# Kernel optimization log

Hardware: AMD Instinct MI355X
Metric: run time of the kernel (lower is better)

## Reference

```python
import jax, jax.numpy as jnp
import numpy as np

N = 100000
H = 512
E = 8
EPS = 1e-12


def _xavier(key, fan_out, fan_in):
    a = float(np.sqrt(6.0 / (fan_in + fan_out)))
    return jax.random.uniform(key, (fan_out, fan_in), jnp.float32, -a, a)


def setup_inputs() -> dict:
    key = jax.random.key(0)
    ks = jax.random.split(key, 5)
    return {
        "x": jax.random.normal(ks[0], (N, H), jnp.float32),
        "Wq": _xavier(ks[1], H, H), "bq": jnp.zeros((H,), jnp.float32),
        "Wk": _xavier(ks[2], H, H), "bk": jnp.zeros((H,), jnp.float32),
        "Wv": _xavier(ks[3], H, H), "bv": jnp.zeros((H,), jnp.float32),
        "We": _xavier(ks[4], E, H), "be": jnp.zeros((E,), jnp.float32),
    }


def reference(x, Wq, bq, Wk, bk, Wv, bv, We, be):
    n = x.shape[0]
    q = x @ Wq.T + bq                      # [N,H]
    k = x @ Wk.T + bk                      # [N,H]
    v = x @ Wv.T + bv                      # [N,H]
    q = q / jnp.maximum(jnp.linalg.norm(q), EPS)   # Frobenius norm scaling
    k = k / jnp.maximum(jnp.linalg.norm(k), EPS)
    k_sum = jnp.sum(k, axis=0)             # k^T @ ones -> [H]
    attn_norm = 1.0 + (q @ k_sum)[:, None] / n     # [N,1]
    kv = k.T @ v                           # [H,H] associative trick
    global_repr = v + (q @ kv) / n         # [N,H]
    global_repr = global_repr / jnp.maximum(attn_norm, EPS)
    global_logits = global_repr @ We.T + be        # [N,E]
    return (global_repr, global_logits)
```

## Files before the change

kernel.cpp:

```cpp
#include <hip/hip_runtime.h>
#include <hip/hip_bf16.h>
#include <stdint.h>

#define Nrows 100000
#define Hdim  512
#define Edim  8


typedef float f32x4 __attribute__((ext_vector_type(4)));
typedef short bfrag __attribute__((ext_vector_type(8)));
typedef unsigned short u16;
typedef unsigned short u16x4 __attribute__((ext_vector_type(4)));

__device__ __forceinline__ u16 f2bf(float f) {
  union { float f; uint32_t u; } v; v.f = f;
  return (u16)((v.u + 0x7FFFu + ((v.u >> 16) & 1u)) >> 16);
}
__device__ __forceinline__ float waveReduce(float p) {
  #pragma unroll
  for (int off = 32; off > 0; off >>= 1) p += __shfl_down(p, off);
  return p;
}
__device__ __forceinline__ int permA(int r) {
  return (r & 1) | ((r & 2) << 1) | ((r & 4) >> 1);
}

__global__ __launch_bounds__(256) void kPrep(
    const float* __restrict__ Wv, const float* __restrict__ bv,
    const float* __restrict__ We, const float* __restrict__ be,
    u16* __restrict__ Bfin, float* __restrict__ b2e) {
  int b = blockIdx.x, t = threadIdx.x, lane = t & 63, wid = t >> 6;
  if (b < 8) {
    __shared__ float wes[512];
    for (int j = t; j < 512; j += 256) wes[j] = We[(size_t)b * Hdim + j];
    __syncthreads();
    float a0 = 0.f, a1 = 0.f;
    for (int j = 0; j < 512; ++j) {
      float w = wes[j];
      a0 += w * Wv[(size_t)j * Hdim + t];
      a1 += w * Wv[(size_t)j * Hdim + t + 256];
    }
    Bfin[(size_t)(512 + b) * Hdim + t]       = f2bf(a0);
    Bfin[(size_t)(512 + b) * Hdim + t + 256] = f2bf(a1);
    if (wid == 0) {
      float p = 0.f;
      for (int j = lane; j < 512; j += 64) p += wes[j] * bv[j];
      p = waveReduce(p);
      if (lane == 0) b2e[512 + b] = p + be[b];
    }
  } else {
    int c = b - 8;
    #pragma unroll 4
    for (int i = 0; i < 32; ++i) {
      int idx = c * 32768 + i * 1024 + t * 4;
      float4 v = *(const float4*)(Wv + idx);
      u16x4 o = { f2bf(v.x), f2bf(v.y), f2bf(v.z), f2bf(v.w) };
      *(u16x4*)(Bfin + idx) = o;
    }
    if (c == 0) { b2e[t] = bv[t]; b2e[t + 256] = bv[t + 256]; }
  }
}

__global__ __launch_bounds__(256, 2) void kMain(
    const float* __restrict__ x, const u16* __restrict__ Bfin,
    const float* __restrict__ b2e, float* __restrict__ out) {
  extern __shared__ char smem[];
  u16* __restrict__ Alds = (u16*)smem;
  u16* __restrict__ Blds = (u16*)(smem + 65536);
  const int t = threadIdx.x, lane = t & 63, wid = t >> 6;
  const int wm = wid >> 1, wc = wid & 1;
  const int l15 = lane & 15, l16 = lane >> 4;
  const int m0 = blockIdx.x * 64;

  const int a_row = t >> 2, a_c = t & 3;
  const int a_perm = permA(a_row);
  int arg = m0 + a_row; if (arg > Nrows - 1) arg = Nrows - 1;
  const float* xrow = x + (size_t)arg * Hdim;

  const int b_row = t >> 1, b_p = t & 1;
  const int b_xor = b_row & 7;

  float4 ra0, ra1, ra2, ra3; bfrag rb0, rb1, rb2, rb3;
  ra0 = *(const float4*)(xrow + a_c * 8);
  ra1 = *(const float4*)(xrow + a_c * 8 + 4);
  ra2 = *(const float4*)(xrow + (a_c + 4) * 8);
  ra3 = *(const float4*)(xrow + (a_c + 4) * 8 + 4);
  {
    const u16* bp = Bfin + (size_t)b_row * Hdim + b_p * 32;
    rb0 = *(const bfrag*)bp;        rb1 = *(const bfrag*)(bp + 8);
    rb2 = *(const bfrag*)(bp + 16); rb3 = *(const bfrag*)(bp + 24);
  }

  f32x4 acc[2][4] = {};
  for (int s = 0; s < 32; ++s) {
    const int nt = s >> 3, kt = s & 7;
    __syncthreads();
    if (nt == 0) {
      bfrag w0, w1;
      w0[0] = (short)f2bf(ra0.x); w0[1] = (short)f2bf(ra0.y);
      w0[2] = (short)f2bf(ra0.z); w0[3] = (short)f2bf(ra0.w);
      w0[4] = (short)f2bf(ra1.x); w0[5] = (short)f2bf(ra1.y);
      w0[6] = (short)f2bf(ra1.z); w0[7] = (short)f2bf(ra1.w);
      w1[0] = (short)f2bf(ra2.x); w1[1] = (short)f2bf(ra2.y);
      w1[2] = (short)f2bf(ra2.z); w1[3] = (short)f2bf(ra2.w);
      w1[4] = (short)f2bf(ra3.x); w1[5] = (short)f2bf(ra3.y);
      w1[6] = (short)f2bf(ra3.z); w1[7] = (short)f2bf(ra3.w);
      *(bfrag*)&Alds[a_row * 512 + (kt * 8 + (a_c ^ a_perm)) * 8] = w0;
      *(bfrag*)&Alds[a_row * 512 + (kt * 8 + ((a_c + 4) ^ a_perm)) * 8] = w1;
    }
    *(bfrag*)&Blds[b_row * 64 + (((b_p * 4 + 0) ^ b_xor) * 8)] = rb0;
    *(bfrag*)&Blds[b_row * 64 + (((b_p * 4 + 1) ^ b_xor) * 8)] = rb1;
    *(bfrag*)&Blds[b_row * 64 + (((b_p * 4 + 2) ^ b_xor) * 8)] = rb2;
    *(bfrag*)&Blds[b_row * 64 + (((b_p * 4 + 3) ^ b_xor) * 8)] = rb3;
    if (s < 31) {
      const int s1 = s + 1, nt1 = s1 >> 3, kt1 = s1 & 7;
      if (s1 < 8) {
        const float* xp = xrow + kt1 * 64;
        ra0 = *(const float4*)(xp + a_c * 8);
        ra1 = *(const float4*)(xp + a_c * 8 + 4);
        ra2 = *(const float4*)(xp + (a_c + 4) * 8);
        ra3 = *(const float4*)(xp + (a_c + 4) * 8 + 4);
      }
      const u16* bp = Bfin + (size_t)(nt1 * 128 + b_row) * Hdim + kt1 * 64 + b_p * 32;
      rb0 = *(const bfrag*)bp;        rb1 = *(const bfrag*)(bp + 8);
      rb2 = *(const bfrag*)(bp + 16); rb3 = *(const bfrag*)(bp + 24);
    }
    __syncthreads();
    #pragma unroll
    for (int ks = 0; ks < 2; ++ks) {
      bfrag af[2], bfr[4];
      #pragma unroll
      for (int mi = 0; mi < 2; ++mi) {
        int r = wm * 32 + mi * 16 + l15;
        af[mi] = *(const bfrag*)&Alds[r * 512 + (kt * 8 + ((ks * 4 + l16) ^ permA(r))) * 8];
      }
      #pragma unroll
      for (int cf = 0; cf < 4; ++cf) {
        int r = wc * 64 + cf * 16 + l15;
        bfr[cf] = *(const bfrag*)&Blds[r * 64 + (((ks * 4 + l16) ^ (r & 7)) * 8)];
      }
      #pragma unroll
      for (int mi = 0; mi < 2; ++mi)
        #pragma unroll
        for (int cf = 0; cf < 4; ++cf)
          acc[mi][cf] = __builtin_amdgcn_mfma_f32_16x16x32_bf16(af[mi], bfr[cf], acc[mi][cf], 0, 0, 0);
    }
    if (kt == 7) {
      #pragma unroll
      for (int cf = 0; cf < 4; ++cf) {
        int col = nt * 128 + wc * 64 + cf * 16 + l15;
        float bias = b2e[col];
        #pragma unroll
        for (int mi = 0; mi < 2; ++mi) {
          #pragma unroll
          for (int r = 0; r < 4; ++r) {
            int n = m0 + wm * 32 + mi * 16 + l16 * 4 + r;
            if (n < Nrows) out[(size_t)n * Hdim + col] = acc[mi][cf][r] + bias;
            acc[mi][cf][r] = 0.f;
          }
        }
      }
    }
  }

  bfrag tb[16];
  #pragma unroll
  for (int i = 0; i < 16; ++i)
    tb[i] = *(const bfrag*)(Bfin + (size_t)(512 + l15) * Hdim + i * 32 + l16 * 8);
  f32x4 acc2 = {};
  const int trow = wid * 16 + l15;
  const int tperm = permA(trow);
  #pragma unroll
  for (int i = 0; i < 16; ++i) {
    int cg = i * 4 + l16;
    bfrag a2 = *(const bfrag*)&Alds[trow * 512 + ((cg & ~7) | ((cg & 7) ^ tperm)) * 8];
    acc2 = __builtin_amdgcn_mfma_f32_16x16x32_bf16(a2, tb[i], acc2, 0, 0, 0);
  }
  if (l15 < 8) {
    float bias = b2e[512 + l15];
    #pragma unroll
    for (int r = 0; r < 4; ++r) {
      int n = m0 + wid * 16 + l16 * 4 + r;
      if (n < Nrows) out[(size_t)Nrows * Hdim + (size_t)n * Edim + l15] = acc2[r] + bias;
    }
  }
}

extern "C" void kernel_launch(void* const* d_in, const int* in_sizes, int n_in,
                              void* d_out, int out_size, void* d_ws, size_t ws_size,
                              hipStream_t stream) {
  const float* x  = (const float*)d_in[0];
  const float* Wv = (const float*)d_in[5];
  const float* bv = (const float*)d_in[6];
  const float* We = (const float*)d_in[7];
  const float* be = (const float*)d_in[8];
  float* out = (float*)d_out;
  char* ws = (char*)d_ws;

  size_t off = 0;
  auto alloc = [&](size_t bytes) { size_t o = off; off += (bytes + 255) & ~(size_t)255; return o; };
  size_t o_Bfin = alloc((size_t)520 * Hdim * 2);
  size_t o_b2e  = alloc(576 * 4);
  if (ws_size < off) return;

  u16*   Bfin = (u16*)(ws + o_Bfin);
  float* b2e  = (float*)(ws + o_b2e);

  hipFuncSetAttribute(reinterpret_cast<const void*>(kMain),
                      hipFuncAttributeMaxDynamicSharedMemorySize, 81920);

  kPrep<<<16, 256, 0, stream>>>(Wv, bv, We, be, Bfin, b2e);
  kMain<<<1563, 256, 81920, stream>>>(x, Bfin, b2e, out);
}
```

Measured before the change: 212.0 us.

## Restructure main GEMM: 32-row tiles, B fragments read directly from global

Each block now handles 32 rows instead of 64. The x tile is converted to bf16 once into a 32KB static LDS buffer. Each wave computes a 128-column slab over the full K, loading B fragments straight from global/L2 instead of staging them through LDS with double buffering. This removes the per-step barriers and the B LDS traffic, and the smaller footprint allows 4 blocks per CU. In exchange, B reuse now relies on L2/L1 caching and each wave holds 64 accumulator registers. Row bounds checks are dropped because 100000 is a multiple of 32.

```diff
diff --git a/kernel.cpp b/kernel.cpp
--- a/kernel.cpp
+++ b/kernel.cpp
@@ -61,127 +61,97 @@
   }
 }
 
-__global__ __launch_bounds__(256, 2) void kMain(
+__global__ __launch_bounds__(256, 4) void kMain(
     const float* __restrict__ x, const u16* __restrict__ Bfin,
     const float* __restrict__ b2e, float* __restrict__ out) {
-  extern __shared__ char smem[];
-  u16* __restrict__ Alds = (u16*)smem;
-  u16* __restrict__ Blds = (u16*)(smem + 65536);
+  __shared__ u16 Alds[32 * 512];
   const int t = threadIdx.x, lane = t & 63, wid = t >> 6;
-  const int wm = wid >> 1, wc = wid & 1;
   const int l15 = lane & 15, l16 = lane >> 4;
-  const int m0 = blockIdx.x * 64;
+  const int m0 = blockIdx.x * 32;
 
-  const int a_row = t >> 2, a_c = t & 3;
-  const int a_perm = permA(a_row);
-  int arg = m0 + a_row; if (arg > Nrows - 1) arg = Nrows - 1;
-  const float* xrow = x + (size_t)arg * Hdim;
+  {
+    const int r = t >> 3, q = t & 7;
+    const int pr = permA(r);
+    const float* xp = x + (size_t)(m0 + r) * Hdim;
+    #pragma unroll
+    for (int half = 0; half < 2; ++half) {
+      float4 f[8];
+      #pragma unroll
+      for (int j = 0; j < 4; ++j) {
+        int cg = q + 8 * (half * 4 + j);
+        f[2 * j]     = *(const float4*)(xp + cg * 8);
+        f[2 * j + 1] = *(const float4*)(xp + cg * 8 + 4);
+      }
+      #pragma unroll
+      for (int j = 0; j < 4; ++j) {
+        int cg = q + 8 * (half * 4 + j);
+        bfrag w;
+        w[0] = (short)f2bf(f[2*j].x);   w[1] = (short)f2bf(f[2*j].y);
+        w[2] = (short)f2bf(f[2*j].z);   w[3] = (short)f2bf(f[2*j].w);
+        w[4] = (short)f2bf(f[2*j+1].x); w[5] = (short)f2bf(f[2*j+1].y);
+        w[6] = (short)f2bf(f[2*j+1].z); w[7] = (short)f2bf(f[2*j+1].w);
+        *(bfrag*)&Alds[r * 512 + ((cg & ~7) | (q ^ pr)) * 8] = w;
+      }
+    }
+  }
+  __syncthreads();
 
-  const int b_row = t >> 1, b_p = t & 1;
-  const int b_xor = b_row & 7;
-
-  float4 ra0, ra1, ra2, ra3; bfrag rb0, rb1, rb2, rb3;
-  ra0 = *(const float4*)(xrow + a_c * 8);
-  ra1 = *(const float4*)(xrow + a_c * 8 + 4);
-  ra2 = *(const float4*)(xrow + (a_c + 4) * 8);
-  ra3 = *(const float4*)(xrow + (a_c + 4) * 8 + 4);
-  {
-    const u16* bp = Bfin + (size_t)b_row * Hdim + b_p * 32;
-    rb0 = *(const bfrag*)bp;        rb1 = *(const bfrag*)(bp + 8);
-    rb2 = *(const bfrag*)(bp + 16); rb3 = *(const bfrag*)(bp + 24);
+  f32x4 acc[2][8] = {};
+  #pragma unroll 1
+  for (int kc = 0; kc < 16; ++kc) {
+    bfrag bf[8];
+    #pragma unroll
+    for (int cf = 0; cf < 8; ++cf)
+      bf[cf] = *(const bfrag*)(Bfin + (size_t)(wid * 128 + cf * 16 + l15) * Hdim + kc * 32 + l16 * 8);
+    bfrag af[2];
+    #pragma unroll
+    for (int mi = 0; mi < 2; ++mi) {
+      int r = mi * 16 + l15;
+      int cg = kc * 4 + l16;
+      af[mi] = *(const bfrag*)&Alds[r * 512 + ((cg & ~7) | ((cg & 7) ^ permA(r))) * 8];
+    }
+    #pragma unroll
+    for (int mi = 0; mi < 2; ++mi)
+      #pragma unroll
+      for (int cf = 0; cf < 8; ++cf)
+        acc[mi][cf] = __builtin_amdgcn_mfma_f32_16x16x32_bf16(af[mi], bf[cf], acc[mi][cf], 0, 0, 0);
   }
 
-  f32x4 acc[2][4] = {};
-  for (int s = 0; s < 32; ++s) {
-    const int nt = s >> 3, kt = s & 7;
-    __syncthreads();
-    if (nt == 0) {
-      bfrag w0, w1;
-      w0[0] = (short)f2bf(ra0.x); w0[1] = (short)f2bf(ra0.y);
-      w0[2] = (short)f2bf(ra0.z); w0[3] = (short)f2bf(ra0.w);
-      w0[4] = (short)f2bf(ra1.x); w0[5] = (short)f2bf(ra1.y);
-      w0[6] = (short)f2bf(ra1.z); w0[7] = (short)f2bf(ra1.w);
-      w1[0] = (short)f2bf(ra2.x); w1[1] = (short)f2bf(ra2.y);
-      w1[2] = (short)f2bf(ra2.z); w1[3] = (short)f2bf(ra2.w);
-      w1[4] = (short)f2bf(ra3.x); w1[5] = (short)f2bf(ra3.y);
-      w1[6] = (short)f2bf(ra3.z); w1[7] = (short)f2bf(ra3.w);
-      *(bfrag*)&Alds[a_row * 512 + (kt * 8 + (a_c ^ a_perm)) * 8] = w0;
-      *(bfrag*)&Alds[a_row * 512 + (kt * 8 + ((a_c + 4) ^ a_perm)) * 8] = w1;
-    }
-    *(bfrag*)&Blds[b_row * 64 + (((b_p * 4 + 0) ^ b_xor) * 8)] = rb0;
-    *(bfrag*)&Blds[b_row * 64 + (((b_p * 4 + 1) ^ b_xor) * 8)] = rb1;
-    *(bfrag*)&Blds[b_row * 64 + (((b_p * 4 + 2) ^ b_xor) * 8)] = rb2;
-    *(bfrag*)&Blds[b_row * 64 + (((b_p * 4 + 3) ^ b_xor) * 8)] = rb3;
-    if (s < 31) {
-      const int s1 = s + 1, nt1 = s1 >> 3, kt1 = s1 & 7;
-      if (s1 < 8) {
-        const float* xp = xrow + kt1 * 64;
-        ra0 = *(const float4*)(xp + a_c * 8);
-        ra1 = *(const float4*)(xp + a_c * 8 + 4);
-        ra2 = *(const float4*)(xp + (a_c + 4) * 8);
-        ra3 = *(const float4*)(xp + (a_c + 4) * 8 + 4);
-      }
-      const u16* bp = Bfin + (size_t)(nt1 * 128 + b_row) * Hdim + kt1 * 64 + b_p * 32;
-      rb0 = *(const bfrag*)bp;        rb1 = *(const bfrag*)(bp + 8);
-      rb2 = *(const bfrag*)(bp + 16); rb3 = *(const bfrag*)(bp + 24);
-    }
-    __syncthreads();
+  #pragma unroll
+  for (int cf = 0; cf < 8; ++cf) {
+    int col = wid * 128 + cf * 16 + l15;
+    float bias = b2e[col];
     #pragma unroll
-    for (int ks = 0; ks < 2; ++ks) {
-      bfrag af[2], bfr[4];
+    for (int mi = 0; mi < 2; ++mi) {
       #pragma unroll
-      for (int mi = 0; mi < 2; ++mi) {
-        int r = wm * 32 + mi * 16 + l15;
-        af[mi] = *(const bfrag*)&Alds[r * 512 + (kt * 8 + ((ks * 4 + l16) ^ permA(r))) * 8];
-      }
-      #pragma unroll
-      for (int cf = 0; cf < 4; ++cf) {
-        int r = wc * 64 + cf * 16 + l15;
-        bfr[cf] = *(const bfrag*)&Blds[r * 64 + (((ks * 4 + l16) ^ (r & 7)) * 8)];
-      }
-      #pragma unroll
-      for (int mi = 0; mi < 2; ++mi)
-        #pragma unroll
-        for (int cf = 0; cf < 4; ++cf)
-          acc[mi][cf] = __builtin_amdgcn_mfma_f32_16x16x32_bf16(af[mi], bfr[cf], acc[mi][cf], 0, 0, 0);
-    }
-    if (kt == 7) {
-      #pragma unroll
-      for (int cf = 0; cf < 4; ++cf) {
-        int col = nt * 128 + wc * 64 + cf * 16 + l15;
-        float bias = b2e[col];
-        #pragma unroll
-        for (int mi = 0; mi < 2; ++mi) {
-          #pragma unroll
-          for (int r = 0; r < 4; ++r) {
-            int n = m0 + wm * 32 + mi * 16 + l16 * 4 + r;
-            if (n < Nrows) out[(size_t)n * Hdim + col] = acc[mi][cf][r] + bias;
-            acc[mi][cf][r] = 0.f;
-          }
-        }
+      for (int r = 0; r < 4; ++r) {
+        int n = m0 + mi * 16 + l16 * 4 + r;
+        out[(size_t)n * Hdim + col] = acc[mi][cf][r] + bias;
       }
     }
   }
 
-  bfrag tb[16];
-  #pragma unroll
-  for (int i = 0; i < 16; ++i)
-    tb[i] = *(const bfrag*)(Bfin + (size_t)(512 + l15) * Hdim + i * 32 + l16 * 8);
-  f32x4 acc2 = {};
-  const int trow = wid * 16 + l15;
-  const int tperm = permA(trow);
-  #pragma unroll
-  for (int i = 0; i < 16; ++i) {
-    int cg = i * 4 + l16;
-    bfrag a2 = *(const bfrag*)&Alds[trow * 512 + ((cg & ~7) | ((cg & 7) ^ tperm)) * 8];
-    acc2 = __builtin_amdgcn_mfma_f32_16x16x32_bf16(a2, tb[i], acc2, 0, 0, 0);
-  }
-  if (l15 < 8) {
-    float bias = b2e[512 + l15];
+  if (wid < 2) {
+    bfrag tb[16];
     #pragma unroll
-    for (int r = 0; r < 4; ++r) {
-      int n = m0 + wid * 16 + l16 * 4 + r;
-      if (n < Nrows) out[(size_t)Nrows * Hdim + (size_t)n * Edim + l15] = acc2[r] + bias;
+    for (int i = 0; i < 16; ++i)
+      tb[i] = *(const bfrag*)(Bfin + (size_t)(512 + l15) * Hdim + i * 32 + l16 * 8);
+    f32x4 acc2 = {};
+    const int trow = wid * 16 + l15;
+    const int tp = permA(trow);
+    #pragma unroll
+    for (int i = 0; i < 16; ++i) {
+      int cg = i * 4 + l16;
+      bfrag a2 = *(const bfrag*)&Alds[trow * 512 + ((cg & ~7) | ((cg & 7) ^ tp)) * 8];
+      acc2 = __builtin_amdgcn_mfma_f32_16x16x32_bf16(a2, tb[i], acc2, 0, 0, 0);
+    }
+    if (l15 < 8) {
+      float bias = b2e[512 + l15];
+      #pragma unroll
+      for (int r = 0; r < 4; ++r) {
+        int n = m0 + wid * 16 + l16 * 4 + r;
+        out[(size_t)Nrows * Hdim + (size_t)n * Edim + l15] = acc2[r] + bias;
+      }
     }
   }
 }
@@ -199,16 +169,13 @@
 
   size_t off = 0;
   auto alloc = [&](size_t bytes) { size_t o = off; off += (bytes + 255) & ~(size_t)255; return o; };
-  size_t o_Bfin = alloc((size_t)520 * Hdim * 2);
+  size_t o_Bfin = alloc((size_t)528 * Hdim * 2);
   size_t o_b2e  = alloc(576 * 4);
   if (ws_size < off) return;
 
   u16*   Bfin = (u16*)(ws + o_Bfin);
   float* b2e  = (float*)(ws + o_b2e);
 
-  hipFuncSetAttribute(reinterpret_cast<const void*>(kMain),
-                      hipFuncAttributeMaxDynamicSharedMemorySize, 81920);
-
   kPrep<<<16, 256, 0, stream>>>(Wv, bv, We, be, Bfin, b2e);
-  kMain<<<1563, 256, 81920, stream>>>(x, Bfin, b2e, out);
+  kMain<<<3125, 256, 0, stream>>>(x, Bfin, b2e, out);
 }
```

Measured after the change: 283.6 us. 33.7% more time.
